# Kernel tuning notes

Hardware: AMD Instinct MI355X
Metric: run time of the kernel (lower is better)

The kernel has to match this reference:

```python
import jax, jax.numpy as jnp
import numpy as np

CODEBOOK_SIZE = 256
EMBED_DIM = 32
N_TOKENS = 524288
EPS = 1e-6


def l2norm(t, eps=EPS):
    # F.normalize(p=2): x / max(||x||, eps)
    n = jnp.sqrt(jnp.sum(t * t, axis=-1, keepdims=True))
    return t / jnp.maximum(n, eps)


def setup_inputs() -> dict:
    key = jax.random.key(0)
    kx, kw = jax.random.split(key)
    x = jax.random.normal(kx, (N_TOKENS, EMBED_DIM), dtype=jnp.float32)
    # embedding.weight.data.uniform_(-1/codebook_size, 1/codebook_size)
    codebook = jax.random.uniform(
        kw, (CODEBOOK_SIZE, EMBED_DIM), dtype=jnp.float32,
        minval=-1.0 / CODEBOOK_SIZE, maxval=1.0 / CODEBOOK_SIZE)
    return {"x": x, "codebook": codebook}


def reference(x, codebook):
    # --- find_nearest_codes: cdist + argmin + gather ---
    # squared euclidean distances have the same argmin as torch.cdist
    x2 = jnp.sum(x * x, axis=-1, keepdims=True)            # [N, 1]
    c2 = jnp.sum(codebook * codebook, axis=-1)             # [K]
    d2 = x2 - 2.0 * (x @ codebook.T) + c2[None, :]         # [N, K]
    indices = jnp.argmin(d2, axis=1)                       # [N] int
    quantized = codebook[indices]                          # [N, D]

    # --- update_usage: histogram over codes ---
    counts = jnp.zeros((CODEBOOK_SIZE,), dtype=jnp.float32).at[indices].add(1.0)

    # --- rotate_to(x, quantized): rotation-trick gradient estimator ---
    u = jax.lax.stop_gradient(l2norm(x))                   # detached direction of src
    q = jax.lax.stop_gradient(l2norm(quantized))           # detached direction of tgt
    w = jax.lax.stop_gradient(l2norm(u + q))               # Householder bisector, detached
    e = x                                                  # gradient flows through e only
    ew = jnp.sum(e * w, axis=-1, keepdims=True)            # (e @ w_col)
    eu = jnp.sum(e * u, axis=-1, keepdims=True)            # (e @ u_col)
    rotated = e - 2.0 * ew * w + 2.0 * eu * q              # [N, D]

    return rotated, indices, counts
```

## Files before the change

### kernel.cpp

```cpp
#include <hip/hip_runtime.h>

#define N_TOK   524288
#define KC      256
#define D       32
#define EPSF    1e-6f
#define TPT     128
#define NTILES  (N_TOK / TPT)
#define NBLK    768
#define BLKT    256

#define WS_HIST_OFF 64

__global__ __launch_bounds__(BLKT, 4) void vq_main(
    const float* __restrict__ x, const float* __restrict__ cb,
    float* __restrict__ out_rot, float* __restrict__ out_idx,
    float* __restrict__ ws, float* __restrict__ out_cnt, int use_ws)
{
    __shared__ float ct[D][KC];
    __shared__ float c2s[KC];
    __shared__ float xt[D][TPT];
    __shared__ float x2s[TPT];
    __shared__ int   bidx[TPT];
    __shared__ float hist[KC];
    __shared__ int   sh_tile;

    const int tid = threadIdx.x;

    {
        const float4* cb4 = (const float4*)(cb + (size_t)tid * D);
#pragma unroll
        for (int j = 0; j < 8; j++) {
            float4 r = cb4[j];
            ct[4 * j + 0][tid] = r.x;
            ct[4 * j + 1][tid] = r.y;
            ct[4 * j + 2][tid] = r.z;
            ct[4 * j + 3][tid] = r.w;
        }
        {
#pragma clang fp contract(off)
            float pr[8];
#pragma unroll
            for (int j = 0; j < 8; j++) {
                float a = ct[j][tid], b = ct[j + 8][tid];
                float c = ct[j + 16][tid], d = ct[j + 24][tid];
                pr[j] = ((a * a + b * b) + c * c) + d * d;
            }
            c2s[tid] = ((pr[0] + pr[1]) + (pr[2] + pr[3])) + ((pr[4] + pr[5]) + (pr[6] + pr[7]));
        }
        hist[tid] = 0.f;
    }
    const int tt = tid >> 4;
    const int tc = tid & 15;

    uint* tile_cnt = (uint*)ws;

    for (int it = 0; ; it++) {
        if (use_ws) { if (tid == 0) sh_tile = (int)atomicAdd(tile_cnt, 1u); }
        __syncthreads();
        const int tile = use_ws ? sh_tile : (blockIdx.x + it * (int)gridDim.x);
        if (tile >= NTILES) break;
        const int tok0 = tile * TPT;

        {
            const float4* xg = (const float4*)(x + (size_t)tok0 * D + (size_t)tid * 16);
            const int tok = tid >> 1;
            const int k0  = (tid & 1) * 16;
#pragma unroll
            for (int j = 0; j < 4; j++) {
                float4 a = xg[j];
                xt[k0 + 4 * j + 0][tok] = a.x;
                xt[k0 + 4 * j + 1][tok] = a.y;
                xt[k0 + 4 * j + 2][tok] = a.z;
                xt[k0 + 4 * j + 3][tok] = a.w;
            }
        }
        __syncthreads();

        if (tid < TPT) {
#pragma clang fp contract(off)
            float pr[8];
#pragma unroll
            for (int j = 0; j < 8; j++) {
                float a = xt[j][tid], b = xt[j + 8][tid];
                float c = xt[j + 16][tid], d = xt[j + 24][tid];
                pr[j] = ((a * a + b * b) + c * c) + d * d;
            }
            x2s[tid] = ((pr[0] + pr[1]) + (pr[2] + pr[3])) + ((pr[4] + pr[5]) + (pr[6] + pr[7]));
        }
        __syncthreads();

        float x8[8];
        {
            float4 xa = *(const float4*)&x2s[tt * 8];
            float4 xb = *(const float4*)&x2s[tt * 8 + 4];
            x8[0] = xa.x; x8[1] = xa.y; x8[2] = xa.z; x8[3] = xa.w;
            x8[4] = xb.x; x8[5] = xb.y; x8[6] = xb.z; x8[7] = xb.w;
        }

        float bestv[8];
        int   besti[8];
#pragma unroll
        for (int i = 0; i < 8; i++) { bestv[i] = 3.4e38f; besti[i] = 0x7fffffff; }

#pragma unroll
        for (int chunk = 0; chunk < 2; chunk++) {
            const int cb0 = chunk * 128 + tc * 4;
            float acc[8][8];
#pragma unroll
            for (int i = 0; i < 8; i++)
#pragma unroll
                for (int j = 0; j < 8; j++) acc[i][j] = 0.f;

#pragma unroll 8
            for (int k = 0; k < D; k++) {
                const float4 xv0 = *(const float4*)&xt[k][tt * 8];
                const float4 xv1 = *(const float4*)&xt[k][tt * 8 + 4];
                const float4 cv0 = *(const float4*)&ct[k][cb0];
                const float4 cv1 = *(const float4*)&ct[k][cb0 + 64];
                const float xs[8] = {xv0.x, xv0.y, xv0.z, xv0.w, xv1.x, xv1.y, xv1.z, xv1.w};
                const float cs[8] = {cv0.x, cv0.y, cv0.z, cv0.w, cv1.x, cv1.y, cv1.z, cv1.w};
#pragma unroll
                for (int i = 0; i < 8; i++)
#pragma unroll
                    for (int j = 0; j < 8; j++)
                        acc[i][j] = __builtin_fmaf(xs[i], cs[j], acc[i][j]);
            }
#pragma unroll
            for (int j = 0; j < 8; j++) {
                const int   cidx = cb0 + ((j < 4) ? j : (60 + j));
                const float c2v  = c2s[cidx];
#pragma unroll
                for (int i = 0; i < 8; i++) {
                    float t2 = x8[i] - 2.0f * acc[i][j];
                    float s  = t2 + c2v;
                    if (s < bestv[i] || (s == bestv[i] && cidx < besti[i])) {
                        bestv[i] = s; besti[i] = cidx;
                    }
                }
            }
        }
#pragma unroll
        for (int m = 1; m < 16; m <<= 1) {
#pragma unroll
            for (int i = 0; i < 8; i++) {
                float ov = __shfl_xor(bestv[i], m, 64);
                int   oi = __shfl_xor(besti[i], m, 64);
                if (ov < bestv[i] || (ov == bestv[i] && oi < besti[i])) {
                    bestv[i] = ov; besti[i] = oi;
                }
            }
        }
        if (tc == 0) {
#pragma unroll
            for (int i = 0; i < 8; i++) bidx[tt * 8 + i] = besti[i];
        }
        __syncthreads();

#pragma unroll
        for (int h = 0; h < 2; h++) {
            const int tok = h * 64 + (tid >> 2);
            const int sub = tid & 3;
            const size_t gtok = (size_t)tok0 + tok;
            const float4* xg = (const float4*)(x + gtok * D + sub * 8);
            float4 xa = xg[0], xb = xg[1];
            const int bi = bidx[tok];
            const float4* cg = (const float4*)(cb + (size_t)bi * D + sub * 8);
            float4 ca = cg[0], cbv = cg[1];

            float xs8[8] = {xa.x, xa.y, xa.z, xa.w, xb.x, xb.y, xb.z, xb.w};
            float cs8[8] = {ca.x, ca.y, ca.z, ca.w, cbv.x, cbv.y, cbv.z, cbv.w};

            float px2 = 0.f, pc2 = 0.f;
#pragma unroll
            for (int j = 0; j < 8; j++) { px2 = fmaf(xs8[j], xs8[j], px2); pc2 = fmaf(cs8[j], cs8[j], pc2); }
            float x2 = px2 + __shfl_xor(px2, 1, 64); x2 += __shfl_xor(x2, 2, 64);
            float c2 = pc2 + __shfl_xor(pc2, 1, 64); c2 += __shfl_xor(c2, 2, 64);
            const float inx = 1.f / fmaxf(sqrtf(x2), EPSF);
            const float inc = 1.f / fmaxf(sqrtf(c2), EPSF);

            float us8[8], qs8[8], ws8[8];
            float pw2 = 0.f;
#pragma unroll
            for (int j = 0; j < 8; j++) {
                us8[j] = xs8[j] * inx;
                qs8[j] = cs8[j] * inc;
                ws8[j] = us8[j] + qs8[j];
                pw2 = fmaf(ws8[j], ws8[j], pw2);
            }
            float w2 = pw2 + __shfl_xor(pw2, 1, 64); w2 += __shfl_xor(w2, 2, 64);
            const float inw = 1.f / fmaxf(sqrtf(w2), EPSF);

            float pew = 0.f, peu = 0.f;
#pragma unroll
            for (int j = 0; j < 8; j++) {
                ws8[j] *= inw;
                pew = fmaf(xs8[j], ws8[j], pew);
                peu = fmaf(xs8[j], us8[j], peu);
            }
            float ew = pew + __shfl_xor(pew, 1, 64); ew += __shfl_xor(ew, 2, 64);
            float eu = peu + __shfl_xor(peu, 1, 64); eu += __shfl_xor(eu, 2, 64);

            float ro[8];
#pragma unroll
            for (int j = 0; j < 8; j++)
                ro[j] = xs8[j] - 2.f * ew * ws8[j] + 2.f * eu * qs8[j];

            float4* og = (float4*)(out_rot + gtok * D + sub * 8);
            og[0] = make_float4(ro[0], ro[1], ro[2], ro[3]);
            og[1] = make_float4(ro[4], ro[5], ro[6], ro[7]);

            if (sub == 0) {
                out_idx[gtok] = (float)bi;
                atomicAdd(&hist[bi], 1.f);
            }
        }
    }

    if (use_ws) ws[WS_HIST_OFF + (size_t)blockIdx.x * KC + tid] = hist[tid];
    else        atomicAdd(&out_cnt[tid], hist[tid]);
}

__global__ __launch_bounds__(256) void vq_reduce(const float* __restrict__ ws,
                                                 float* __restrict__ out_cnt)
{
    const int c = blockIdx.x * 8 + (threadIdx.x >> 5);
    const int l = threadIdx.x & 31;
    float s = 0.f;
    for (int b = l; b < NBLK; b += 32) s += ws[WS_HIST_OFF + (size_t)b * KC + c];
#pragma unroll
    for (int m = 1; m < 32; m <<= 1) s += __shfl_xor(s, m, 64);
    if (l == 0) out_cnt[c] = s;
}

extern "C" void kernel_launch(void* const* d_in, const int* in_sizes, int n_in,
                              void* d_out, int out_size, void* d_ws, size_t ws_size,
                              hipStream_t stream)
{
    const float* x  = (const float*)d_in[0];
    const float* cb = (const float*)d_in[1];
    float* out      = (float*)d_out;
    float* out_rot  = out;
    float* out_idx  = out + (size_t)N_TOK * D;
    float* out_cnt  = out_idx + N_TOK;

    const size_t ws_need = (WS_HIST_OFF + (size_t)NBLK * KC) * sizeof(float);
    const int use_ws = (ws_size >= ws_need) ? 1 : 0;
    if (use_ws) {
        hipMemsetAsync(d_ws, 0, WS_HIST_OFF * sizeof(float), stream);
    } else {
        hipMemsetAsync(out_cnt, 0, KC * sizeof(float), stream);
    }

    vq_main<<<NBLK, BLKT, 0, stream>>>(x, cb, out_rot, out_idx,
                                       (float*)d_ws, out_cnt, use_ws);
    if (use_ws) vq_reduce<<<32, 256, 0, stream>>>((const float*)d_ws, out_cnt);
}
```

Baseline: 252.6 us.

## Screen codebook distances with bf16 MFMA and rescore near-minimum candidates in fp32

Replaces the fp32 register-tiled distance GEMM with per-wave bf16 MFMA 16x16x32 tiles against a padded bf16 codebook copy in shared memory. Each wave handles 16 tokens and no longer needs block-wide barriers per tile. Any code whose approximate score falls within a fixed margin of the row minimum is rescored with an exact fp32 dot product read from global memory, which keeps the argmin exact. The cost is a data-dependent, divergent rescoring path whose work grows with how many candidates fall inside the margin.

```diff
diff --git a/kernel.cpp b/kernel.cpp
--- a/kernel.cpp
+++ b/kernel.cpp
@@ -4,166 +4,182 @@
 #define KC      256
 #define D       32
 #define EPSF    1e-6f
-#define TPT     128
-#define NTILES  (N_TOK / TPT)
-#define NBLK    768
+#define GPW     16
+#define NGRP    (N_TOK / GPW)
+#define NBLK    1024
 #define BLKT    256
-
+#define DELTA   0.008f
+#define FINF    3.4e38f
 #define WS_HIST_OFF 64
+
+typedef __attribute__((ext_vector_type(8))) short bf16x8;
+typedef __attribute__((ext_vector_type(4))) float f32x4;
+
+__device__ inline short f32_bf16_rne(float f) {
+    unsigned u = __float_as_uint(f);
+    u = (u + 0x7fffu + ((u >> 16) & 1u)) >> 16;
+    return (short)u;
+}
 
 __global__ __launch_bounds__(BLKT, 4) void vq_main(
     const float* __restrict__ x, const float* __restrict__ cb,
     float* __restrict__ out_rot, float* __restrict__ out_idx,
     float* __restrict__ ws, float* __restrict__ out_cnt, int use_ws)
 {
-    __shared__ float ct[D][KC];
+    __shared__ short cbb[KC * 40];
     __shared__ float c2s[KC];
-    __shared__ float xt[D][TPT];
-    __shared__ float x2s[TPT];
-    __shared__ int   bidx[TPT];
     __shared__ float hist[KC];
-    __shared__ int   sh_tile;
-
-    const int tid = threadIdx.x;
+
+    const int tid  = threadIdx.x;
+    const int lane = tid & 63;
+    const int wv   = tid >> 6;
+    const int m    = lane & 15;
+    const int q    = lane >> 4;
 
     {
         const float4* cb4 = (const float4*)(cb + (size_t)tid * D);
+        float4 r[8];
+#pragma unroll
+        for (int j = 0; j < 8; j++) r[j] = cb4[j];
+        {
+#pragma clang fp contract(off)
+            float t[32];
+#pragma unroll
+            for (int j = 0; j < 8; j++) {
+                t[4 * j + 0] = r[j].x * r[j].x;
+                t[4 * j + 1] = r[j].y * r[j].y;
+                t[4 * j + 2] = r[j].z * r[j].z;
+                t[4 * j + 3] = r[j].w * r[j].w;
+            }
+            float pr[8];
+#pragma unroll
+            for (int j = 0; j < 8; j++)
+                pr[j] = ((t[j] + t[j + 8]) + t[j + 16]) + t[j + 24];
+            c2s[tid] = ((pr[0] + pr[1]) + (pr[2] + pr[3])) + ((pr[4] + pr[5]) + (pr[6] + pr[7]));
+        }
 #pragma unroll
         for (int j = 0; j < 8; j++) {
-            float4 r = cb4[j];
-            ct[4 * j + 0][tid] = r.x;
-            ct[4 * j + 1][tid] = r.y;
-            ct[4 * j + 2][tid] = r.z;
-            ct[4 * j + 3][tid] = r.w;
-        }
+            cbb[tid * 40 + 4 * j + 0] = f32_bf16_rne(r[j].x);
+            cbb[tid * 40 + 4 * j + 1] = f32_bf16_rne(r[j].y);
+            cbb[tid * 40 + 4 * j + 2] = f32_bf16_rne(r[j].z);
+            cbb[tid * 40 + 4 * j + 3] = f32_bf16_rne(r[j].w);
+        }
+        hist[tid] = 0.f;
+    }
+    __syncthreads();
+
+    uint* cnt = (uint*)ws;
+
+    for (int it = 0;; it++) {
+        int g;
+        if (use_ws) {
+            int v = 0;
+            if (lane == 0) v = (int)atomicAdd(cnt, 1u);
+            g = __shfl(v, 0, 64);
+        } else {
+            g = (blockIdx.x * 4 + wv) + it * (int)gridDim.x * 4;
+        }
+        if (g >= NGRP) break;
+        const int t0 = g * GPW;
+
+        float xr[8];
+        {
+            const float4* xp = (const float4*)(x + (size_t)(t0 + m) * D + q * 8);
+            float4 a = xp[0], b = xp[1];
+            xr[0] = a.x; xr[1] = a.y; xr[2] = a.z; xr[3] = a.w;
+            xr[4] = b.x; xr[5] = b.y; xr[6] = b.z; xr[7] = b.w;
+        }
+        bf16x8 af;
+#pragma unroll
+        for (int j = 0; j < 8; j++) af[j] = f32_bf16_rne(xr[j]);
+
+        float x2b[4];
         {
 #pragma clang fp contract(off)
             float pr[8];
 #pragma unroll
             for (int j = 0; j < 8; j++) {
-                float a = ct[j][tid], b = ct[j + 8][tid];
-                float c = ct[j + 16][tid], d = ct[j + 24][tid];
-                pr[j] = ((a * a + b * b) + c * c) + d * d;
-            }
-            c2s[tid] = ((pr[0] + pr[1]) + (pr[2] + pr[3])) + ((pr[4] + pr[5]) + (pr[6] + pr[7]));
-        }
-        hist[tid] = 0.f;
-    }
-    const int tt = tid >> 4;
-    const int tc = tid & 15;
-
-    uint* tile_cnt = (uint*)ws;
-
-    for (int it = 0; ; it++) {
-        if (use_ws) { if (tid == 0) sh_tile = (int)atomicAdd(tile_cnt, 1u); }
-        __syncthreads();
-        const int tile = use_ws ? sh_tile : (blockIdx.x + it * (int)gridDim.x);
-        if (tile >= NTILES) break;
-        const int tok0 = tile * TPT;
-
-        {
-            const float4* xg = (const float4*)(x + (size_t)tok0 * D + (size_t)tid * 16);
-            const int tok = tid >> 1;
-            const int k0  = (tid & 1) * 16;
-#pragma unroll
-            for (int j = 0; j < 4; j++) {
-                float4 a = xg[j];
-                xt[k0 + 4 * j + 0][tok] = a.x;
-                xt[k0 + 4 * j + 1][tok] = a.y;
-                xt[k0 + 4 * j + 2][tok] = a.z;
-                xt[k0 + 4 * j + 3][tok] = a.w;
-            }
-        }
-        __syncthreads();
-
-        if (tid < TPT) {
-#pragma clang fp contract(off)
-            float pr[8];
-#pragma unroll
-            for (int j = 0; j < 8; j++) {
-                float a = xt[j][tid], b = xt[j + 8][tid];
-                float c = xt[j + 16][tid], d = xt[j + 24][tid];
-                pr[j] = ((a * a + b * b) + c * c) + d * d;
-            }
-            x2s[tid] = ((pr[0] + pr[1]) + (pr[2] + pr[3])) + ((pr[4] + pr[5]) + (pr[6] + pr[7]));
-        }
-        __syncthreads();
-
-        float x8[8];
-        {
-            float4 xa = *(const float4*)&x2s[tt * 8];
-            float4 xb = *(const float4*)&x2s[tt * 8 + 4];
-            x8[0] = xa.x; x8[1] = xa.y; x8[2] = xa.z; x8[3] = xa.w;
-            x8[4] = xb.x; x8[5] = xb.y; x8[6] = xb.z; x8[7] = xb.w;
-        }
-
-        float bestv[8];
-        int   besti[8];
-#pragma unroll
-        for (int i = 0; i < 8; i++) { bestv[i] = 3.4e38f; besti[i] = 0x7fffffff; }
-
-#pragma unroll
-        for (int chunk = 0; chunk < 2; chunk++) {
-            const int cb0 = chunk * 128 + tc * 4;
-            float acc[8][8];
-#pragma unroll
-            for (int i = 0; i < 8; i++)
-#pragma unroll
-                for (int j = 0; j < 8; j++) acc[i][j] = 0.f;
-
-#pragma unroll 8
-            for (int k = 0; k < D; k++) {
-                const float4 xv0 = *(const float4*)&xt[k][tt * 8];
-                const float4 xv1 = *(const float4*)&xt[k][tt * 8 + 4];
-                const float4 cv0 = *(const float4*)&ct[k][cb0];
-                const float4 cv1 = *(const float4*)&ct[k][cb0 + 64];
-                const float xs[8] = {xv0.x, xv0.y, xv0.z, xv0.w, xv1.x, xv1.y, xv1.z, xv1.w};
-                const float cs[8] = {cv0.x, cv0.y, cv0.z, cv0.w, cv1.x, cv1.y, cv1.z, cv1.w};
-#pragma unroll
-                for (int i = 0; i < 8; i++)
-#pragma unroll
-                    for (int j = 0; j < 8; j++)
-                        acc[i][j] = __builtin_fmaf(xs[i], cs[j], acc[i][j]);
-            }
-#pragma unroll
-            for (int j = 0; j < 8; j++) {
-                const int   cidx = cb0 + ((j < 4) ? j : (60 + j));
-                const float c2v  = c2s[cidx];
-#pragma unroll
-                for (int i = 0; i < 8; i++) {
-                    float t2 = x8[i] - 2.0f * acc[i][j];
-                    float s  = t2 + c2v;
-                    if (s < bestv[i] || (s == bestv[i] && cidx < besti[i])) {
-                        bestv[i] = s; besti[i] = cidx;
+                float sq  = xr[j] * xr[j];
+                float s16 = __shfl_xor(sq, 16, 64);
+                float s32 = __shfl_xor(sq, 32, 64);
+                float s48 = __shfl_xor(sq, 48, 64);
+                pr[j] = ((sq + s16) + s32) + s48;
+            }
+            float x2tok = ((pr[0] + pr[1]) + (pr[2] + pr[3])) + ((pr[4] + pr[5]) + (pr[6] + pr[7]));
+#pragma unroll
+            for (int r = 0; r < 4; r++)
+                x2b[r] = __shfl(x2tok, q * 4 + r, 64);
+        }
+
+        const f32x4 accz = {0.f, 0.f, 0.f, 0.f};
+        float sc[16][4];
+        float minv4[4] = {FINF, FINF, FINF, FINF};
+#pragma unroll
+        for (int t = 0; t < 16; t++) {
+            bf16x8 bfr = *(const bf16x8*)&cbb[(t * 16 + m) * 40 + q * 8];
+            float  c2v = c2s[t * 16 + m];
+            f32x4  acc = __builtin_amdgcn_mfma_f32_16x16x32_bf16(af, bfr, accz, 0, 0, 0);
+#pragma unroll
+            for (int r = 0; r < 4; r++) {
+                float s = fmaf(-2.f, acc[r], c2v);
+                sc[t][r] = s;
+                minv4[r] = fminf(minv4[r], s);
+            }
+        }
+#pragma unroll
+        for (int mm = 1; mm < 16; mm <<= 1)
+#pragma unroll
+            for (int r = 0; r < 4; r++)
+                minv4[r] = fminf(minv4[r], __shfl_xor(minv4[r], mm, 64));
+
+        float bestE[4] = {FINF, FINF, FINF, FINF};
+        int   bestI[4] = {0x7fffffff, 0x7fffffff, 0x7fffffff, 0x7fffffff};
+#pragma unroll
+        for (int t = 0; t < 16; t++) {
+#pragma unroll
+            for (int r = 0; r < 4; r++) {
+                if (sc[t][r] <= minv4[r] + DELTA) {
+                    const int    code = t * 16 + m;
+                    const size_t tok  = (size_t)t0 + q * 4 + r;
+                    const float4* xp = (const float4*)(x + tok * D);
+                    const float4* cp = (const float4*)(cb + (size_t)code * D);
+                    float acc = 0.f;
+#pragma unroll
+                    for (int c = 0; c < 8; c++) {
+                        float4 a = xp[c], b = cp[c];
+                        acc = fmaf(a.x, b.x, acc);
+                        acc = fmaf(a.y, b.y, acc);
+                        acc = fmaf(a.z, b.z, acc);
+                        acc = fmaf(a.w, b.w, acc);
+                    }
+                    float t2 = x2b[r] - 2.0f * acc;
+                    float s2 = t2 + c2s[code];
+                    if (s2 < bestE[r] || (s2 == bestE[r] && code < bestI[r])) {
+                        bestE[r] = s2; bestI[r] = code;
                     }
                 }
             }
         }
 #pragma unroll
-        for (int m = 1; m < 16; m <<= 1) {
-#pragma unroll
-            for (int i = 0; i < 8; i++) {
-                float ov = __shfl_xor(bestv[i], m, 64);
-                int   oi = __shfl_xor(besti[i], m, 64);
-                if (ov < bestv[i] || (ov == bestv[i] && oi < besti[i])) {
-                    bestv[i] = ov; besti[i] = oi;
+        for (int mm = 1; mm < 16; mm <<= 1)
+#pragma unroll
+            for (int r = 0; r < 4; r++) {
+                float ov = __shfl_xor(bestE[r], mm, 64);
+                int   oi = __shfl_xor(bestI[r], mm, 64);
+                if (ov < bestE[r] || (ov == bestE[r] && oi < bestI[r])) {
+                    bestE[r] = ov; bestI[r] = oi;
                 }
             }
-        }
-        if (tc == 0) {
-#pragma unroll
-            for (int i = 0; i < 8; i++) bidx[tt * 8 + i] = besti[i];
-        }
-        __syncthreads();
-
-#pragma unroll
-        for (int h = 0; h < 2; h++) {
-            const int tok = h * 64 + (tid >> 2);
-            const int sub = tid & 3;
-            const size_t gtok = (size_t)tok0 + tok;
+
+        {
+            const int tl  = lane >> 2;
+            const int sub = lane & 3;
+            const int r   = tl & 3;
+            int bi = (r == 0) ? bestI[0] : (r == 1) ? bestI[1] : (r == 2) ? bestI[2] : bestI[3];
+            const size_t gtok = (size_t)t0 + tl;
+
             const float4* xg = (const float4*)(x + gtok * D + sub * 8);
             float4 xa = xg[0], xb = xg[1];
-            const int bi = bidx[tok];
             const float4* cg = (const float4*)(cb + (size_t)bi * D + sub * 8);
             float4 ca = cg[0], cbv = cg[1];
 
@@ -216,6 +232,7 @@
         }
     }
 
+    __syncthreads();
     if (use_ws) ws[WS_HIST_OFF + (size_t)blockIdx.x * KC + tid] = hist[tid];
     else        atomicAdd(&out_cnt[tid], hist[tid]);
 }
@@ -228,7 +245,7 @@
     float s = 0.f;
     for (int b = l; b < NBLK; b += 32) s += ws[WS_HIST_OFF + (size_t)b * KC + c];
 #pragma unroll
-    for (int m = 1; m < 32; m <<= 1) s += __shfl_xor(s, m, 64);
+    for (int mm = 1; mm < 32; mm <<= 1) s += __shfl_xor(s, mm, 64);
     if (l == 0) out_cnt[c] = s;
 }
 
```

After: 689.6 us. 173% more time.
